# Kernel optimization log

Hardware: AMD Instinct MI355X
Metric: run time of the kernel (lower is better)

The kernel has to match this reference:

```python
import jax, jax.numpy as jnp
import numpy as np

L = 4      # number of layers (graph nodes)
B = 128    # batch
H = 4096   # neurons per layer


def setup_inputs() -> dict:
    key = jax.random.key(0)
    k1, k2, k3 = jax.random.split(key, 3)
    # per-layer source activations, stacked: [L, B, H]
    states = jax.random.normal(k1, (L, B, H), dtype=jnp.float32)
    # all Connection weight matrices, W[t, s] maps source s -> target t: [L, L, H_out, H_in]
    # scaled by 1/sqrt(H) so summed matmuls stay O(1) (original uses constant w_init)
    W = jax.random.normal(k2, (L, L, H, H), dtype=jnp.float32) * (1.0 / np.sqrt(H))
    # external inputs added into each target's current: [L, B, H]
    ext = jax.random.normal(k3, (L, B, H), dtype=jnp.float32)
    return {"states": states, "W": W, "ext": ext}


def reference(states, W, ext):
    # Synapses/Links: for each target t, sum over sources s of (x_s @ W[t,s].T)
    # (Connection.forward is x @ w.T). Single fused einsum replaces the
    # jit.fork fan-out over L*L small matmuls + Python-level sum.
    currents = jnp.einsum('sbh,tsoh->tbo', states, W) + ext  # [L, B, H]
    # Layer/Neurons: per-node activation function
    return jnp.tanh(currents)
```

## Files before the change

### kernel.cpp

```cpp
#include <hip/hip_runtime.h>
#include <hip/hip_bf16.h>
#include <stdint.h>

#define L_ 4
#define B_ 128
#define H_ 4096
#define BK 64
#define BN 32
#define NTHR 256
#define NTOT (L_*B_*H_)
#define ABYTES (128*BK*2)
#define WBYTES (BN*BK*2)
#define BUFB   (ABYTES+WBYTES)

typedef _Float16 f16x8 __attribute__((ext_vector_type(8)));
typedef float    f32x4 __attribute__((ext_vector_type(4)));
typedef float    f4    __attribute__((ext_vector_type(4)));
typedef uint32_t u32x4 __attribute__((ext_vector_type(4)));
typedef uint32_t u32x2 __attribute__((ext_vector_type(2)));

__device__ __forceinline__ uint32_t pack2(float a, float b) {
  const _Float16 ha = (_Float16)a;
  const _Float16 hb = (_Float16)b;
  const uint32_t ua = (uint32_t)__builtin_bit_cast(uint16_t, ha);
  const uint32_t ub = (uint32_t)__builtin_bit_cast(uint16_t, hb);
  return ua | (ub << 16);
}

__global__ void cvt_states_kernel(const float* __restrict__ x,
                                  uint32_t* __restrict__ y, int n4) {
  const int i = blockIdx.x * blockDim.x + threadIdx.x;
  if (i < n4) {
    f4 v = reinterpret_cast<const f4*>(x)[i];
    u32x2 o;
    o.x = pack2(v.x, v.y);
    o.y = pack2(v.z, v.w);
    reinterpret_cast<u32x2*>(y)[i] = o;
  }
}

__device__ __forceinline__ void bar_lgkm0() {
  __builtin_amdgcn_sched_barrier(0);
  asm volatile("s_waitcnt lgkmcnt(0)");
  __builtin_amdgcn_sched_barrier(0);
  __builtin_amdgcn_s_barrier();
  __builtin_amdgcn_sched_barrier(0);
}

template<int SPLIT>
__global__ __launch_bounds__(NTHR, 2*SPLIT)
void net_gemm_kernel(const uint16_t* __restrict__ statesh,
                     const float* __restrict__ Wm,
                     const float* __restrict__ ext,
                     float* __restrict__ out,
                     float* __restrict__ part)
{
  constexpr int KITN = 256 / SPLIT;
  __shared__ __align__(16) uint8_t lds[2 * BUFB];

  const int tid  = threadIdx.x;
  const int bid  = blockIdx.x;
  const int n0   = (bid & 127) * BN;
  const int t    = (bid >> 7) & 3;
  const int kh   = bid >> 9;
  const int sbase = kh * (L_ / SPLIT);

  const int wv   = tid >> 6;
  const int lane = tid & 63;
  const int lid  = lane & 15;
  const int lh   = lane >> 4;

  const int arow = tid >> 3;
  const int acol = (tid & 7) * 8;
  const uint32_t a_st_off =
      (uint32_t)arow * 128 + (((uint32_t)(tid & 7) * 16) ^ ((uint32_t)(arow & 7) << 4));
  const uint16_t* ah_base = statesh + (size_t)arow * H_ + acol;

  const int wrow = tid >> 4;
  const int wcol = (tid & 15) * 4;
  const float* w_base = Wm + ((size_t)t * L_ * H_ + (size_t)(n0 + wrow)) * H_ + wcol;
  const uint32_t w_st0 =
      (uint32_t)ABYTES + (uint32_t)wrow * 128 + (((uint32_t)(tid & 15) * 8) ^ ((uint32_t)(wrow & 7) << 4));
  const uint32_t w_st1 = w_st0 + 16 * 128;

  uint32_t a_rd[2][2], b_rd[2][2];
  #pragma unroll
  for (int mf = 0; mf < 2; ++mf)
    #pragma unroll
    for (int kk = 0; kk < 2; ++kk) {
      const int row = wv * 32 + mf * 16 + lid;
      a_rd[mf][kk] = (uint32_t)row * 128 +
                     (((uint32_t)(kk * 64 + lh * 16)) ^ ((uint32_t)(lid & 7) << 4));
    }
  #pragma unroll
  for (int nf = 0; nf < 2; ++nf)
    #pragma unroll
    for (int kk = 0; kk < 2; ++kk) {
      const int row = nf * 16 + lid;
      b_rd[nf][kk] = (uint32_t)ABYTES + (uint32_t)row * 128 +
                     (((uint32_t)(kk * 64 + lh * 16)) ^ ((uint32_t)(lid & 7) << 4));
    }

  f32x4 acc[2][2] = {};

  u32x4 ah0[4], ah1[4];
  f4    wf0[2], wf1[2];

  auto LOADg = [&](int kidx, u32x4 (&ah)[4], f4 (&wf)[2]) {
    const int s  = sbase + (kidx >> 6);
    const int h0 = (kidx & 63) << 6;
    const uint16_t* ap = ah_base + (size_t)s * (B_ * H_) + h0;
    #pragma unroll
    for (int j = 0; j < 4; ++j)
      ah[j] = *reinterpret_cast<const u32x4*>(ap + (size_t)j * (32 * H_));
    const float* wp = w_base + (size_t)s * ((size_t)H_ * H_) + h0;
    wf[0] = __builtin_nontemporal_load(reinterpret_cast<const f4*>(wp));
    wf[1] = __builtin_nontemporal_load(reinterpret_cast<const f4*>(wp + 16 * (size_t)H_));
  };

  auto WRITEg = [&](uint8_t* base, u32x4 (&ah)[4], f4 (&wf)[2]) {
    #pragma unroll
    for (int j = 0; j < 4; ++j)
      *reinterpret_cast<u32x4*>(base + j * 4096 + a_st_off) = ah[j];
    u32x2 w0, w1;
    w0.x = pack2(wf[0].x, wf[0].y); w0.y = pack2(wf[0].z, wf[0].w);
    w1.x = pack2(wf[1].x, wf[1].y); w1.y = pack2(wf[1].z, wf[1].w);
    *reinterpret_cast<u32x2*>(base + w_st0) = w0;
    *reinterpret_cast<u32x2*>(base + w_st1) = w1;
  };

  auto COMPUTE = [&](const uint8_t* base) {
    f16x8 av[2][2], bv[2][2];
    #pragma unroll
    for (int mf = 0; mf < 2; ++mf)
      #pragma unroll
      for (int kk = 0; kk < 2; ++kk)
        av[mf][kk] = *reinterpret_cast<const f16x8*>(base + a_rd[mf][kk]);
    #pragma unroll
    for (int nf = 0; nf < 2; ++nf)
      #pragma unroll
      for (int kk = 0; kk < 2; ++kk)
        bv[nf][kk] = *reinterpret_cast<const f16x8*>(base + b_rd[nf][kk]);
    #pragma unroll
    for (int kk = 0; kk < 2; ++kk)
      #pragma unroll
      for (int mf = 0; mf < 2; ++mf)
        #pragma unroll
        for (int nf = 0; nf < 2; ++nf)
          acc[mf][nf] = __builtin_amdgcn_mfma_f32_16x16x32_f16(
              av[mf][kk], bv[nf][kk], acc[mf][nf], 0, 0, 0);
  };

  uint8_t* buf0 = lds;
  uint8_t* buf1 = lds + BUFB;

  LOADg(0, ah0, wf0);
  LOADg(1, ah1, wf1);
  WRITEg(buf0, ah0, wf0);
  bar_lgkm0();

  #pragma unroll 1
  for (int k = 0; k < KITN; k += 2) {
    if (k + 2 < KITN) LOADg(k + 2, ah0, wf0);
    COMPUTE(buf0);
    WRITEg(buf1, ah1, wf1);
    bar_lgkm0();

    if (k + 3 < KITN) LOADg(k + 3, ah1, wf1);
    COMPUTE(buf1);
    if (k + 2 < KITN) {
      WRITEg(buf0, ah0, wf0);
      bar_lgkm0();
    }
  }

  #pragma unroll
  for (int mf = 0; mf < 2; ++mf)
    #pragma unroll
    for (int nf = 0; nf < 2; ++nf)
      #pragma unroll
      for (int j = 0; j < 4; ++j) {
        const int brow = wv * 32 + mf * 16 + lh * 4 + j;
        const int ocol = n0 + nf * 16 + lid;
        const size_t idx = ((size_t)(t * B_ + brow)) * H_ + ocol;
        if constexpr (SPLIT == 1) {
          out[idx] = tanhf(acc[mf][nf][j] + ext[idx]);
        } else {
          float* pb = part + (size_t)kh * NTOT;
          __builtin_nontemporal_store(acc[mf][nf][j], &pb[idx]);
        }
      }
}

__global__ __launch_bounds__(NTHR)
void reduce_kernel(const float* __restrict__ part,
                   const float* __restrict__ ext,
                   float* __restrict__ out)
{
  const int i = blockIdx.x * blockDim.x + threadIdx.x;
  f4 p0 = __builtin_nontemporal_load(reinterpret_cast<const f4*>(part) + i);
  f4 p1 = __builtin_nontemporal_load(reinterpret_cast<const f4*>(part + NTOT) + i);
  f4 e  = reinterpret_cast<const f4*>(ext)[i];
  f4 r;
  r.x = tanhf(p0.x + p1.x + e.x);
  r.y = tanhf(p0.y + p1.y + e.y);
  r.z = tanhf(p0.z + p1.z + e.z);
  r.w = tanhf(p0.w + p1.w + e.w);
  reinterpret_cast<f4*>(out)[i] = r;
}

__global__ __launch_bounds__(NTHR, 2)
void net_gemm_fb(const float* __restrict__ statesf,
                 const float* __restrict__ Wm,
                 const float* __restrict__ ext,
                 float* __restrict__ out)
{
  __shared__ __align__(16) uint8_t lds[2 * BUFB];

  const int tid  = threadIdx.x;
  const int bid  = blockIdx.x;
  const int t    = bid >> 7;
  const int n0   = (bid & 127) * BN;
  const int wv   = tid >> 6;
  const int lane = tid & 63;
  const int lid  = lane & 15;
  const int lh   = lane >> 4;

  const int arow = tid >> 3;
  const int acol = (tid & 7) * 8;
  const uint32_t a_st_off =
      (uint32_t)arow * 128 + (((uint32_t)(tid & 7) * 16) ^ ((uint32_t)(arow & 7) << 4));
  const float* af_base = statesf + (size_t)arow * H_ + acol;

  const int wrow = tid >> 4;
  const int wcol = (tid & 15) * 4;
  const float* w_base = Wm + ((size_t)t * L_ * H_ + (size_t)(n0 + wrow)) * H_ + wcol;
  const uint32_t w_st0 =
      (uint32_t)ABYTES + (uint32_t)wrow * 128 + (((uint32_t)(tid & 15) * 8) ^ ((uint32_t)(wrow & 7) << 4));
  const uint32_t w_st1 = w_st0 + 16 * 128;

  uint32_t a_rd[2][2], b_rd[2][2];
  #pragma unroll
  for (int mf = 0; mf < 2; ++mf)
    #pragma unroll
    for (int kk = 0; kk < 2; ++kk) {
      const int row = wv * 32 + mf * 16 + lid;
      a_rd[mf][kk] = (uint32_t)row * 128 +
                     (((uint32_t)(kk * 64 + lh * 16)) ^ ((uint32_t)(lid & 7) << 4));
    }
  #pragma unroll
  for (int nf = 0; nf < 2; ++nf)
    #pragma unroll
    for (int kk = 0; kk < 2; ++kk) {
      const int row = nf * 16 + lid;
      b_rd[nf][kk] = (uint32_t)ABYTES + (uint32_t)row * 128 +
                     (((uint32_t)(kk * 64 + lh * 16)) ^ ((uint32_t)(lid & 7) << 4));
    }

  f32x4 acc[2][2] = {};
  f4 af0[4][2], af1[4][2], wf0[2], wf1[2];

  auto LOADg = [&](int kidx, f4 (&af)[4][2], f4 (&wfx)[2]) {
    const int s  = kidx >> 6;
    const int h0 = (kidx & 63) << 6;
    const float* ap = af_base + (size_t)s * (B_ * H_) + h0;
    #pragma unroll
    for (int j = 0; j < 4; ++j) {
      af[j][0] = *reinterpret_cast<const f4*>(ap + (size_t)j * (32 * H_));
      af[j][1] = *reinterpret_cast<const f4*>(ap + (size_t)j * (32 * H_) + 4);
    }
    const float* wp = w_base + (size_t)s * ((size_t)H_ * H_) + h0;
    wfx[0] = __builtin_nontemporal_load(reinterpret_cast<const f4*>(wp));
    wfx[1] = __builtin_nontemporal_load(reinterpret_cast<const f4*>(wp + 16 * (size_t)H_));
  };

  auto WRITEg = [&](uint8_t* base, f4 (&af)[4][2], f4 (&wfx)[2]) {
    #pragma unroll
    for (int j = 0; j < 4; ++j) {
      u32x4 v;
      v.x = pack2(af[j][0].x, af[j][0].y);
      v.y = pack2(af[j][0].z, af[j][0].w);
      v.z = pack2(af[j][1].x, af[j][1].y);
      v.w = pack2(af[j][1].z, af[j][1].w);
      *reinterpret_cast<u32x4*>(base + j * 4096 + a_st_off) = v;
    }
    u32x2 w0, w1;
    w0.x = pack2(wfx[0].x, wfx[0].y); w0.y = pack2(wfx[0].z, wfx[0].w);
    w1.x = pack2(wfx[1].x, wfx[1].y); w1.y = pack2(wfx[1].z, wfx[1].w);
    *reinterpret_cast<u32x2*>(base + w_st0) = w0;
    *reinterpret_cast<u32x2*>(base + w_st1) = w1;
  };

  auto COMPUTE = [&](const uint8_t* base) {
    f16x8 av[2][2], bv[2][2];
    #pragma unroll
    for (int mf = 0; mf < 2; ++mf)
      #pragma unroll
      for (int kk = 0; kk < 2; ++kk)
        av[mf][kk] = *reinterpret_cast<const f16x8*>(base + a_rd[mf][kk]);
    #pragma unroll
    for (int nf = 0; nf < 2; ++nf)
      #pragma unroll
      for (int kk = 0; kk < 2; ++kk)
        bv[nf][kk] = *reinterpret_cast<const f16x8*>(base + b_rd[nf][kk]);
    #pragma unroll
    for (int kk = 0; kk < 2; ++kk)
      #pragma unroll
      for (int mf = 0; mf < 2; ++mf)
        #pragma unroll
        for (int nf = 0; nf < 2; ++nf)
          acc[mf][nf] = __builtin_amdgcn_mfma_f32_16x16x32_f16(
              av[mf][kk], bv[nf][kk], acc[mf][nf], 0, 0, 0);
  };

  uint8_t* buf0 = lds;
  uint8_t* buf1 = lds + BUFB;

  LOADg(0, af0, wf0);
  LOADg(1, af1, wf1);
  WRITEg(buf0, af0, wf0);
  bar_lgkm0();

  #pragma unroll 1
  for (int k = 0; k < 256; k += 2) {
    if (k + 2 < 256) LOADg(k + 2, af0, wf0);
    COMPUTE(buf0);
    WRITEg(buf1, af1, wf1);
    bar_lgkm0();
    if (k + 3 < 256) LOADg(k + 3, af1, wf1);
    COMPUTE(buf1);
    if (k + 2 < 256) {
      WRITEg(buf0, af0, wf0);
      bar_lgkm0();
    }
  }

  #pragma unroll
  for (int mf = 0; mf < 2; ++mf)
    #pragma unroll
    for (int nf = 0; nf < 2; ++nf)
      #pragma unroll
      for (int j = 0; j < 4; ++j) {
        const int brow = wv * 32 + mf * 16 + lh * 4 + j;
        const int ocol = n0 + nf * 16 + lid;
        const size_t idx = ((size_t)(t * B_ + brow)) * H_ + ocol;
        out[idx] = tanhf(acc[mf][nf][j] + ext[idx]);
      }
}

extern "C" void kernel_launch(void* const* d_in, const int* in_sizes, int n_in,
                              void* d_out, int out_size, void* d_ws, size_t ws_size,
                              hipStream_t stream) {
  const float* states = (const float*)d_in[0];
  const float* W      = (const float*)d_in[1];
  const float* ext    = (const float*)d_in[2];
  float* out          = (float*)d_out;

  const size_t st_bytes   = (size_t)NTOT * 2;
  const size_t part_bytes = (size_t)2 * NTOT * 4;
  const int n4 = NTOT / 4;

  if (ws_size >= st_bytes + part_bytes) {
    float* part = (float*)((uint8_t*)d_ws + st_bytes);
    cvt_states_kernel<<<n4 / 256, NTHR, 0, stream>>>(states, (uint32_t*)d_ws, n4);
    net_gemm_kernel<2><<<1024, NTHR, 0, stream>>>(
        (const uint16_t*)d_ws, W, ext, out, part);
    reduce_kernel<<<n4 / 256, NTHR, 0, stream>>>(part, ext, out);
  } else if (ws_size >= st_bytes) {
    cvt_states_kernel<<<n4 / 256, NTHR, 0, stream>>>(states, (uint32_t*)d_ws, n4);
    net_gemm_kernel<1><<<512, NTHR, 0, stream>>>(
        (const uint16_t*)d_ws, W, ext, out, nullptr);
  } else {
    net_gemm_fb<<<512, NTHR, 0, stream>>>(states, W, ext, out);
  }
}
```

Baseline: 257.1 us.

## Pretile states into MFMA fragment layout, load A directly to registers, drop split-K

States are converted to fp16 in a layout matching MFMA fragments so each wave reads its A operands straight from global memory into registers with triple buffering, leaving only W staged through LDS. The split-K path and its reduction kernel are removed, so one GEMM kernel with 512 blocks does the full K loop and fuses bias plus tanh. This removes the partial-sum write/read traffic and LDS traffic for A, at the cost of fewer blocks in flight and per-wave L2 reads of A.

```diff
diff --git a/kernel.cpp b/kernel.cpp
--- a/kernel.cpp
+++ b/kernel.cpp
@@ -7,11 +7,10 @@
 #define H_ 4096
 #define BK 64
 #define BN 32
+#define KIT 256
 #define NTHR 256
 #define NTOT (L_*B_*H_)
-#define ABYTES (128*BK*2)
 #define WBYTES (BN*BK*2)
-#define BUFB   (ABYTES+WBYTES)
 
 typedef _Float16 f16x8 __attribute__((ext_vector_type(8)));
 typedef float    f32x4 __attribute__((ext_vector_type(4)));
@@ -27,16 +26,23 @@
   return ua | (ub << 16);
 }
 
-__global__ void cvt_states_kernel(const float* __restrict__ x,
-                                  uint32_t* __restrict__ y, int n4) {
-  const int i = blockIdx.x * blockDim.x + threadIdx.x;
-  if (i < n4) {
-    f4 v = reinterpret_cast<const f4*>(x)[i];
-    u32x2 o;
-    o.x = pack2(v.x, v.y);
-    o.y = pack2(v.z, v.w);
-    reinterpret_cast<u32x2*>(y)[i] = o;
-  }
+__global__ __launch_bounds__(NTHR)
+void cvt_tile_kernel(const float* __restrict__ x, u32x4* __restrict__ ws)
+{
+  const int d   = blockIdx.x * NTHR + threadIdx.x;
+  const int row = d & 127;
+  const int lh  = (d >> 7) & 3;
+  const int kk  = (d >> 9) & 1;
+  const int kt  = d >> 10;
+  const int s   = kt >> 6;
+  const int kb  = kt & 63;
+  const float* src = x + ((size_t)(s * B_ + row)) * H_ + kb * 64 + kk * 32 + lh * 8;
+  f4 lo = *reinterpret_cast<const f4*>(src);
+  f4 hi = *reinterpret_cast<const f4*>(src + 4);
+  u32x4 v;
+  v.x = pack2(lo.x, lo.y); v.y = pack2(lo.z, lo.w);
+  v.z = pack2(hi.x, hi.y); v.w = pack2(hi.z, hi.w);
+  ws[d] = v;
 }
 
 __device__ __forceinline__ void bar_lgkm0() {
@@ -47,95 +53,74 @@
   __builtin_amdgcn_sched_barrier(0);
 }
 
-template<int SPLIT>
-__global__ __launch_bounds__(NTHR, 2*SPLIT)
-void net_gemm_kernel(const uint16_t* __restrict__ statesh,
+__global__ __launch_bounds__(NTHR, 2)
+void net_gemm_kernel(const uint8_t* __restrict__ atiled,
                      const float* __restrict__ Wm,
                      const float* __restrict__ ext,
-                     float* __restrict__ out,
-                     float* __restrict__ part)
+                     float* __restrict__ out)
 {
-  constexpr int KITN = 256 / SPLIT;
-  __shared__ __align__(16) uint8_t lds[2 * BUFB];
+  __shared__ __align__(16) uint8_t lds[2 * WBYTES];
 
   const int tid  = threadIdx.x;
   const int bid  = blockIdx.x;
+  const int t    = bid >> 7;
   const int n0   = (bid & 127) * BN;
-  const int t    = (bid >> 7) & 3;
-  const int kh   = bid >> 9;
-  const int sbase = kh * (L_ / SPLIT);
 
   const int wv   = tid >> 6;
   const int lane = tid & 63;
   const int lid  = lane & 15;
   const int lh   = lane >> 4;
 
-  const int arow = tid >> 3;
-  const int acol = (tid & 7) * 8;
-  const uint32_t a_st_off =
-      (uint32_t)arow * 128 + (((uint32_t)(tid & 7) * 16) ^ ((uint32_t)(arow & 7) << 4));
-  const uint16_t* ah_base = statesh + (size_t)arow * H_ + acol;
+  const uint8_t* a_base = atiled + lh * 2048 + (wv * 32 + lid) * 16;
 
   const int wrow = tid >> 4;
   const int wcol = (tid & 15) * 4;
   const float* w_base = Wm + ((size_t)t * L_ * H_ + (size_t)(n0 + wrow)) * H_ + wcol;
   const uint32_t w_st0 =
-      (uint32_t)ABYTES + (uint32_t)wrow * 128 + (((uint32_t)(tid & 15) * 8) ^ ((uint32_t)(wrow & 7) << 4));
+      (uint32_t)wrow * 128 + (((uint32_t)(tid & 15) * 8) ^ ((uint32_t)(wrow & 7) << 4));
   const uint32_t w_st1 = w_st0 + 16 * 128;
 
-  uint32_t a_rd[2][2], b_rd[2][2];
-  #pragma unroll
-  for (int mf = 0; mf < 2; ++mf)
-    #pragma unroll
-    for (int kk = 0; kk < 2; ++kk) {
-      const int row = wv * 32 + mf * 16 + lid;
-      a_rd[mf][kk] = (uint32_t)row * 128 +
-                     (((uint32_t)(kk * 64 + lh * 16)) ^ ((uint32_t)(lid & 7) << 4));
-    }
+  uint32_t b_rd[2][2];
   #pragma unroll
   for (int nf = 0; nf < 2; ++nf)
     #pragma unroll
     for (int kk = 0; kk < 2; ++kk) {
       const int row = nf * 16 + lid;
-      b_rd[nf][kk] = (uint32_t)ABYTES + (uint32_t)row * 128 +
+      b_rd[nf][kk] = (uint32_t)row * 128 +
                      (((uint32_t)(kk * 64 + lh * 16)) ^ ((uint32_t)(lid & 7) << 4));
     }
 
   f32x4 acc[2][2] = {};
 
-  u32x4 ah0[4], ah1[4];
+  f16x8 aS0[2][2], aS1[2][2], aS2[2][2];
   f4    wf0[2], wf1[2];
 
-  auto LOADg = [&](int kidx, u32x4 (&ah)[4], f4 (&wf)[2]) {
-    const int s  = sbase + (kidx >> 6);
+  auto LOADA = [&](int kt, f16x8 (&a)[2][2]) {
+    const uint8_t* p = a_base + (size_t)kt * 16384;
+    a[0][0] = *reinterpret_cast<const f16x8*>(p);
+    a[1][0] = *reinterpret_cast<const f16x8*>(p + 256);
+    a[0][1] = *reinterpret_cast<const f16x8*>(p + 8192);
+    a[1][1] = *reinterpret_cast<const f16x8*>(p + 8192 + 256);
+  };
+
+  auto LOADW = [&](int kidx, f4 (&w)[2]) {
+    const int s  = kidx >> 6;
     const int h0 = (kidx & 63) << 6;
-    const uint16_t* ap = ah_base + (size_t)s * (B_ * H_) + h0;
-    #pragma unroll
-    for (int j = 0; j < 4; ++j)
-      ah[j] = *reinterpret_cast<const u32x4*>(ap + (size_t)j * (32 * H_));
     const float* wp = w_base + (size_t)s * ((size_t)H_ * H_) + h0;
-    wf[0] = __builtin_nontemporal_load(reinterpret_cast<const f4*>(wp));
-    wf[1] = __builtin_nontemporal_load(reinterpret_cast<const f4*>(wp + 16 * (size_t)H_));
-  };
-
-  auto WRITEg = [&](uint8_t* base, u32x4 (&ah)[4], f4 (&wf)[2]) {
-    #pragma unroll
-    for (int j = 0; j < 4; ++j)
-      *reinterpret_cast<u32x4*>(base + j * 4096 + a_st_off) = ah[j];
+    w[0] = __builtin_nontemporal_load(reinterpret_cast<const f4*>(wp));
+    w[1] = __builtin_nontemporal_load(reinterpret_cast<const f4*>(wp + 16 * (size_t)H_));
+  };
+
+  auto WRITEW = [&](uint8_t* base, f4 (&w)[2]) {
     u32x2 w0, w1;
-    w0.x = pack2(wf[0].x, wf[0].y); w0.y = pack2(wf[0].z, wf[0].w);
-    w1.x = pack2(wf[1].x, wf[1].y); w1.y = pack2(wf[1].z, wf[1].w);
+    w0.x = pack2(w[0].x, w[0].y); w0.y = pack2(w[0].z, w[0].w);
+    w1.x = pack2(w[1].x, w[1].y); w1.y = pack2(w[1].z, w[1].w);
     *reinterpret_cast<u32x2*>(base + w_st0) = w0;
     *reinterpret_cast<u32x2*>(base + w_st1) = w1;
   };
 
-  auto COMPUTE = [&](const uint8_t* base) {
-    f16x8 av[2][2], bv[2][2];
-    #pragma unroll
-    for (int mf = 0; mf < 2; ++mf)
-      #pragma unroll
-      for (int kk = 0; kk < 2; ++kk)
-        av[mf][kk] = *reinterpret_cast<const f16x8*>(base + a_rd[mf][kk]);
+  auto COMPUTE = [&](const uint8_t* base, f16x8 (&av)[2][2]) {
+    f16x8 bv[2][2];
     #pragma unroll
     for (int nf = 0; nf < 2; ++nf)
       #pragma unroll
@@ -152,27 +137,39 @@
   };
 
   uint8_t* buf0 = lds;
-  uint8_t* buf1 = lds + BUFB;
-
-  LOADg(0, ah0, wf0);
-  LOADg(1, ah1, wf1);
-  WRITEg(buf0, ah0, wf0);
+  uint8_t* buf1 = lds + WBYTES;
+
+  LOADW(0, wf0);
+  LOADW(1, wf1);
+  LOADA(0, aS0);
+  LOADA(1, aS1);
+  WRITEW(buf0, wf0);
   bar_lgkm0();
 
+  #define BODY(j_, AL_, AU_, WL_, WW_, BU_, BW_) do { \
+      LOADA((j_) + 2, AL_);                           \
+      LOADW((j_) + 2, WL_);                           \
+      COMPUTE(BU_, AU_);                              \
+      WRITEW(BW_, WW_);                               \
+      bar_lgkm0();                                    \
+    } while (0)
+
   #pragma unroll 1
-  for (int k = 0; k < KITN; k += 2) {
-    if (k + 2 < KITN) LOADg(k + 2, ah0, wf0);
-    COMPUTE(buf0);
-    WRITEg(buf1, ah1, wf1);
-    bar_lgkm0();
-
-    if (k + 3 < KITN) LOADg(k + 3, ah1, wf1);
-    COMPUTE(buf1);
-    if (k + 2 < KITN) {
-      WRITEg(buf0, ah0, wf0);
-      bar_lgkm0();
-    }
+  for (int k = 0; k < 252; k += 6) {
+    BODY(k + 0, aS2, aS0, wf0, wf1, buf0, buf1);
+    BODY(k + 1, aS0, aS1, wf1, wf0, buf1, buf0);
+    BODY(k + 2, aS1, aS2, wf0, wf1, buf0, buf1);
+    BODY(k + 3, aS2, aS0, wf1, wf0, buf1, buf0);
+    BODY(k + 4, aS0, aS1, wf0, wf1, buf0, buf1);
+    BODY(k + 5, aS1, aS2, wf1, wf0, buf1, buf0);
   }
+  BODY(252, aS2, aS0, wf0, wf1, buf0, buf1);
+  BODY(253, aS0, aS1, wf1, wf0, buf1, buf0);
+  COMPUTE(buf0, aS2);
+  WRITEW(buf1, wf1);
+  bar_lgkm0();
+  COMPUTE(buf1, aS0);
+  #undef BODY
 
   #pragma unroll
   for (int mf = 0; mf < 2; ++mf)
@@ -183,39 +180,19 @@
         const int brow = wv * 32 + mf * 16 + lh * 4 + j;
         const int ocol = n0 + nf * 16 + lid;
         const size_t idx = ((size_t)(t * B_ + brow)) * H_ + ocol;
-        if constexpr (SPLIT == 1) {
-          out[idx] = tanhf(acc[mf][nf][j] + ext[idx]);
-        } else {
-          float* pb = part + (size_t)kh * NTOT;
-          __builtin_nontemporal_store(acc[mf][nf][j], &pb[idx]);
-        }
+        out[idx] = tanhf(acc[mf][nf][j] + ext[idx]);
       }
 }
 
-__global__ __launch_bounds__(NTHR)
-void reduce_kernel(const float* __restrict__ part,
-                   const float* __restrict__ ext,
-                   float* __restrict__ out)
-{
-  const int i = blockIdx.x * blockDim.x + threadIdx.x;
-  f4 p0 = __builtin_nontemporal_load(reinterpret_cast<const f4*>(part) + i);
-  f4 p1 = __builtin_nontemporal_load(reinterpret_cast<const f4*>(part + NTOT) + i);
-  f4 e  = reinterpret_cast<const f4*>(ext)[i];
-  f4 r;
-  r.x = tanhf(p0.x + p1.x + e.x);
-  r.y = tanhf(p0.y + p1.y + e.y);
-  r.z = tanhf(p0.z + p1.z + e.z);
-  r.w = tanhf(p0.w + p1.w + e.w);
-  reinterpret_cast<f4*>(out)[i] = r;
-}
-
+#define FB_ABYTES (128*BK*2)
+#define FB_BUFB   (FB_ABYTES+WBYTES)
 __global__ __launch_bounds__(NTHR, 2)
 void net_gemm_fb(const float* __restrict__ statesf,
                  const float* __restrict__ Wm,
                  const float* __restrict__ ext,
                  float* __restrict__ out)
 {
-  __shared__ __align__(16) uint8_t lds[2 * BUFB];
+  __shared__ __align__(16) uint8_t lds[2 * FB_BUFB];
 
   const int tid  = threadIdx.x;
   const int bid  = blockIdx.x;
@@ -236,7 +213,7 @@
   const int wcol = (tid & 15) * 4;
   const float* w_base = Wm + ((size_t)t * L_ * H_ + (size_t)(n0 + wrow)) * H_ + wcol;
   const uint32_t w_st0 =
-      (uint32_t)ABYTES + (uint32_t)wrow * 128 + (((uint32_t)(tid & 15) * 8) ^ ((uint32_t)(wrow & 7) << 4));
+      (uint32_t)FB_ABYTES + (uint32_t)wrow * 128 + (((uint32_t)(tid & 15) * 8) ^ ((uint32_t)(wrow & 7) << 4));
   const uint32_t w_st1 = w_st0 + 16 * 128;
 
   uint32_t a_rd[2][2], b_rd[2][2];
@@ -253,7 +230,7 @@
     #pragma unroll
     for (int kk = 0; kk < 2; ++kk) {
       const int row = nf * 16 + lid;
-      b_rd[nf][kk] = (uint32_t)ABYTES + (uint32_t)row * 128 +
+      b_rd[nf][kk] = (uint32_t)FB_ABYTES + (uint32_t)row * 128 +
                      (((uint32_t)(kk * 64 + lh * 16)) ^ ((uint32_t)(lid & 7) << 4));
     }
 
@@ -314,7 +291,7 @@
   };
 
   uint8_t* buf0 = lds;
-  uint8_t* buf1 = lds + BUFB;
+  uint8_t* buf1 = lds + FB_BUFB;
 
   LOADg(0, af0, wf0);
   LOADg(1, af1, wf1);
@@ -356,20 +333,12 @@
   const float* ext    = (const float*)d_in[2];
   float* out          = (float*)d_out;
 
-  const size_t st_bytes   = (size_t)NTOT * 2;
-  const size_t part_bytes = (size_t)2 * NTOT * 4;
-  const int n4 = NTOT / 4;
-
-  if (ws_size >= st_bytes + part_bytes) {
-    float* part = (float*)((uint8_t*)d_ws + st_bytes);
-    cvt_states_kernel<<<n4 / 256, NTHR, 0, stream>>>(states, (uint32_t*)d_ws, n4);
-    net_gemm_kernel<2><<<1024, NTHR, 0, stream>>>(
-        (const uint16_t*)d_ws, W, ext, out, part);
-    reduce_kernel<<<n4 / 256, NTHR, 0, stream>>>(part, ext, out);
-  } else if (ws_size >= st_bytes) {
-    cvt_states_kernel<<<n4 / 256, NTHR, 0, stream>>>(states, (uint32_t*)d_ws, n4);
-    net_gemm_kernel<1><<<512, NTHR, 0, stream>>>(
-        (const uint16_t*)d_ws, W, ext, out, nullptr);
+  const size_t st_bytes = (size_t)NTOT * 2;
+  if (ws_size >= st_bytes) {
+    const int nunits = NTOT / 8;
+    cvt_tile_kernel<<<nunits / NTHR, NTHR, 0, stream>>>(states, (u32x4*)d_ws);
+    net_gemm_kernel<<<512, NTHR, 0, stream>>>(
+        (const uint8_t*)d_ws, W, ext, out);
   } else {
     net_gemm_fb<<<512, NTHR, 0, stream>>>(states, W, ext, out);
   }
```

Result: faster. 242.8 us (-5.6%).
